# Kernel optimization log

Hardware: AMD Instinct MI355X
Metric: run time of the kernel (lower is better)

The kernel has to match this reference:

```python
import jax, jax.numpy as jnp
import numpy as np

SIZE = 784          # number of MPS sites (pixels)
D = 32              # bond dimension
EMB_D = 2           # local feature dim, embedding x -> [1-x, x]
NUM_LABELS = 10
LABEL_SITE = SIZE // 2
BATCH = 128
INIT_STD = 0.01     # matches default 'random_eye' init


def setup_inputs() -> dict:
    key = jax.random.key(0)
    k1, k2, k3 = jax.random.split(key, 3)
    # raw pixel values in [0,1] so the affine embedding is valid
    batch_input = jax.random.uniform(k1, (BATCH, SIZE), dtype=jnp.float32)
    eye = jnp.eye(D, dtype=jnp.float32)
    # 'random_eye' init: identity (broadcast over site & physical dims) + small noise.
    # Keeps the 784-long matrix chain numerically well-conditioned.
    core_tensors = eye[None, :, None, :] + INIT_STD * jax.random.normal(
        k2, (SIZE, D, EMB_D, D), dtype=jnp.float32)
    label_tensor = eye[:, None, :] + INIT_STD * jax.random.normal(
        k3, (D, NUM_LABELS, D), dtype=jnp.float32)
    return {"batch_input": batch_input,
            "core_tensors": core_tensors,
            "label_tensor": label_tensor}


def _chain_matmul(mats):
    """Ordered product M_0 @ M_1 @ ... @ M_{n-1} via log-depth pairwise tree.
    mats: [B, n, D, D] -> [B, D, D]. n is static, so the Python while is fine."""
    while mats.shape[1] > 1:
        n = mats.shape[1]
        half = n // 2
        prod = jnp.matmul(mats[:, 0:2 * half:2], mats[:, 1:2 * half:2])
        if n % 2:
            prod = jnp.concatenate([prod, mats[:, -1:]], axis=1)
        mats = prod
    return mats[:, 0]


def reference(batch_input, core_tensors, label_tensor):
    # embedding_map: x -> [1-x, x]                                  [B, S, d]
    emb = jnp.stack([1.0 - batch_input, batch_input], axis=-1)
    # _contract_batch_input: per-site matrices M[b,s] = sum_d core[s,:,d,:]*emb[b,s,d]
    mats = jnp.einsum('sadc,bsd->bsac', core_tensors, emb)       # [B, S, D, D]
    left = _chain_matmul(mats[:, :LABEL_SITE])                    # [B, D, D]
    right = _chain_matmul(mats[:, LABEL_SITE:])                   # [B, D, D]
    # periodic bc: out[b,l] = trace(left @ T_l @ right)
    return jnp.einsum('bij,jlk,bki->bl', left, label_tensor, right)  # [B, num_labels]
```

## Files before the change

kernel.cpp:

```cpp
#include <hip/hip_runtime.h>
#include <stdint.h>

typedef float f32x16 __attribute__((ext_vector_type(16)));
typedef short bf16x8 __attribute__((ext_vector_type(8)));
typedef uint32_t u32;
typedef uint32_t u32x4 __attribute__((ext_vector_type(4)));

#define SIZE 784
#define NLBL 10
#define LABEL_SITE 392
#define BATCH 128
#define PRE_ELEMS (SIZE * 2 * 64 * 4)


__device__ inline u32 cvt_pk(float a, float b) {
  u32 r;
  asm("v_cvt_pk_bf16_f32 %0, %1, %2" : "=v"(r) : "v"(a), "v"(b));
  return r;
}
__device__ inline float lo16f(u32 h) { return __uint_as_float(h << 16); }
__device__ inline float hi16f(u32 h) { return __uint_as_float(h & 0xffff0000u); }

__device__ inline void split_pack(const float s[8], u32 hi[4], u32 lo[4]) {
#pragma unroll
  for (int p = 0; p < 4; ++p) {
    u32 h = cvt_pk(s[2 * p], s[2 * p + 1]);
    hi[p] = h;
    lo[p] = cvt_pk(s[2 * p] - lo16f(h), s[2 * p + 1] - hi16f(h));
  }
}

__device__ inline f32x16 mfma_bb(const u32 (&a)[4], const u32 (&b)[4], f32x16 c) {
  union U { u32 u[4]; bf16x8 v; };
  U A, B;
#pragma unroll
  for (int i = 0; i < 4; ++i) { A.u[i] = a[i]; B.u[i] = b[i]; }
  return __builtin_amdgcn_mfma_f32_32x32x16_bf16(A.v, B.v, c, 0, 0, 0);
}
__device__ inline f32x16 mfma_v4(u32x4 a, const u32 (&b)[4], f32x16 c) {
  union UA { u32x4 u; bf16x8 v; } A; A.u = a;
  union UB { u32 u[4]; bf16x8 v; } B;
#pragma unroll
  for (int i = 0; i < 4; ++i) B.u[i] = b[i];
  return __builtin_amdgcn_mfma_f32_32x32x16_bf16(A.v, B.v, c, 0, 0, 0);
}

__device__ inline f32x16 ident_acc(int lane) {
  const int gam = lane & 31, hib = lane >> 5;
  f32x16 a;
#pragma unroll
  for (int reg = 0; reg < 16; ++reg) {
    int rho = (reg & 3) + 8 * (reg >> 2) + 4 * hib;
    a[reg] = (rho == gam) ? 1.0f : 0.0f;
  }
  return a;
}

__device__ inline void build_b(const f32x16& acc, int hib, int t,
                               u32 (&Bh)[4], u32 (&Bl)[4]) {
  float slot[8];
#pragma unroll
  for (int j = 0; j < 4; ++j) {
    const int q1 = 8 * t + j, q2 = q1 + 4;
    float z = hib ? acc[q1] : acc[q2];
    float wv = __shfl_xor(z, 32, 64);
    slot[j]     = hib ? wv : acc[q1];
    slot[j + 4] = hib ? acc[q2] : wv;
  }
  split_pack(slot, Bh, Bl);
}

__device__ inline f32x16 chain_step(const u32 (&Ah)[2][4], const u32 (&Al)[2][4],
                                    f32x16 acc, int hib) {
  f32x16 r;
#pragma unroll
  for (int q = 0; q < 16; ++q) r[q] = 0.0f;
#pragma unroll
  for (int t = 0; t < 2; ++t) {
    u32 Bh[4], Bl[4];
    build_b(acc, hib, t, Bh, Bl);
    r = mfma_bb(Al[t], Bh, r);
    r = mfma_bb(Ah[t], Bl, r);
    r = mfma_bb(Ah[t], Bh, r);
  }
  return r;
}

__device__ inline void store_afrag(float* dst, f32x16 acc, int lane) {
  const int gam = lane & 31, hib = lane >> 5;
  const int h = gam >> 4, j = gam & 7, b5 = (gam >> 3) & 1;
#pragma unroll
  for (int reg = 0; reg < 16; ++reg) {
    int rho = (reg & 3) + 8 * (reg >> 2) + 4 * hib;
    int lp = rho + 32 * b5;
    dst[h * 512 + lp * 8 + j] = acc[reg];
  }
}

__device__ inline void load_split_afrag(const float* src, int lane,
                                        u32 (&Ah)[2][4], u32 (&Al)[2][4]) {
#pragma unroll
  for (int h = 0; h < 2; ++h) {
    const float4* p = (const float4*)(src + h * 512 + lane * 8);
    float4 q0 = p[0], q1 = p[1];
    float v[8] = {q0.x, q0.y, q0.z, q0.w, q1.x, q1.y, q1.z, q1.w};
    split_pack(v, Ah[h], Al[h]);
  }
}

__global__ __launch_bounds__(256) void mps_precomp(const float* __restrict__ core,
                                                   u32* __restrict__ pc0h,
                                                   u32* __restrict__ pc0l,
                                                   u32* __restrict__ pdh,
                                                   u32* __restrict__ pdl) {
  const int tid = threadIdx.x;
  const int w = tid >> 6, lane = tid & 63;
  const int task = blockIdx.x * 4 + w;
  const int s = task >> 1, t = task & 1;
  const int r = lane & 31, hib = lane >> 5;
  const float* cs = core + (size_t)s * 2048 + r;
  u32 wc0h[4], wc0l[4], wdh[4], wdl[4];
#pragma unroll
  for (int p = 0; p < 4; ++p) {
    const int k0 = 16 * t + 8 * hib + 2 * p;
    float a0 = cs[k0 * 64],       a1 = cs[(k0 + 1) * 64];
    float b0 = cs[k0 * 64 + 32],  b1 = cs[(k0 + 1) * 64 + 32];
    float d0 = b0 - a0, d1 = b1 - a1;
    u32 h = cvt_pk(a0, a1);
    wc0h[p] = h;
    wc0l[p] = cvt_pk(a0 - lo16f(h), a1 - hi16f(h));
    u32 gg = cvt_pk(d0, d1);
    wdh[p] = gg;
    wdl[p] = cvt_pk(d0 - lo16f(gg), d1 - hi16f(gg));
  }
  const size_t base = ((size_t)task * 64 + lane) * 4;
  *(u32x4*)(pc0h + base) = *(u32x4*)wc0h;
  *(u32x4*)(pc0l + base) = *(u32x4*)wc0l;
  *(u32x4*)(pdh  + base) = *(u32x4*)wdh;
  *(u32x4*)(pdl  + base) = *(u32x4*)wdl;
}

__global__ __launch_bounds__(256, 4) void mps_phase1(
    const float* __restrict__ input,
    const u32* __restrict__ pc0h, const u32* __restrict__ pc0l,
    const u32* __restrict__ pdh,  const u32* __restrict__ pdl,
    float* __restrict__ wsA, int nseg, int seglen) {
  const int tid = threadIdx.x;
  const int w = tid >> 6, lane = tid & 63;
  const int hib = lane >> 5;
  const int g = blockIdx.x % nseg, c = blockIdx.x / nseg;
  const int bi = c * 4 + w;

  f32x16 acc = ident_acc(lane);
  f32x16 z16;
#pragma unroll
  for (int q = 0; q < 16; ++q) z16[q] = 0.0f;

  const int ci0 = g * seglen;
  for (int i = 0; i < seglen; ++i) {
    int s = LABEL_SITE + ci0 + i;
    if (s >= SIZE) s -= SIZE;
    const float x = input[(size_t)bi * SIZE + s];
    f32x16 rc = z16, rd = z16;
#pragma unroll
    for (int t = 0; t < 2; ++t) {
      const size_t base = ((size_t)(s * 2 + t) * 64 + lane) * 4;
      u32x4 Ac0h = *(const u32x4*)(pc0h + base);
      u32x4 Ac0l = *(const u32x4*)(pc0l + base);
      u32x4 Adh  = *(const u32x4*)(pdh + base);
      u32x4 Adl  = *(const u32x4*)(pdl + base);
      u32 Bh[4], Bl[4];
      build_b(acc, hib, t, Bh, Bl);
      rd = mfma_v4(Adl, Bh, rd);
      rd = mfma_v4(Adh, Bl, rd);
      rd = mfma_v4(Adh, Bh, rd);
      rc = mfma_v4(Ac0l, Bh, rc);
      rc = mfma_v4(Ac0h, Bl, rc);
      rc = mfma_v4(Ac0h, Bh, rc);
    }
#pragma unroll
    for (int q = 0; q < 16; ++q) acc[q] = fmaf(x, rd[q], rc[q]);
  }
  store_afrag(wsA + ((size_t)bi * nseg + g) * 1024, acc, lane);
}

__global__ __launch_bounds__(256) void mps_phase2a(const float* __restrict__ wsA,
                                                   float* __restrict__ wsB,
                                                   int nseg, int GG) {
  const int tid = threadIdx.x;
  const int w = tid >> 6, lane = tid & 63;
  const int wid = blockIdx.x * 4 + w;
  const int bi = wid & 127, gg = wid >> 7;
  f32x16 acc = ident_acc(lane);
  for (int g = gg * GG; g < gg * GG + GG; ++g) {
    u32 Ah[2][4], Al[2][4];
    load_split_afrag(wsA + ((size_t)bi * nseg + g) * 1024, lane, Ah, Al);
    acc = chain_step(Ah, Al, acc, lane >> 5);
  }
  store_afrag(wsB + ((size_t)bi * 7 + gg) * 1024, acc, lane);
}

__global__ __launch_bounds__(256) void mps_phase2b(const float* __restrict__ wsB,
                                                   const float* __restrict__ label,
                                                   float* __restrict__ out) {
  const int tid = threadIdx.x;
  const int w = tid >> 6, lane = tid & 63;
  const int bi = blockIdx.x * 4 + w;
  const int gam = lane & 31, hib = lane >> 5;
  f32x16 acc = ident_acc(lane);
  for (int gg = 0; gg < 7; ++gg) {
    u32 Ah[2][4], Al[2][4];
    load_split_afrag(wsB + ((size_t)bi * 7 + gg) * 1024, lane, Ah, Al);
    acc = chain_step(Ah, Al, acc, hib);
  }
  float part[NLBL];
#pragma unroll
  for (int l = 0; l < NLBL; ++l) part[l] = 0.0f;
#pragma unroll
  for (int reg = 0; reg < 16; ++reg) {
    const int rho = (reg & 3) + 8 * (reg >> 2) + 4 * hib;
    const float wv = acc[reg];
    const float* tp = label + rho * (NLBL * 32) + gam;
#pragma unroll
    for (int l = 0; l < NLBL; ++l) part[l] = fmaf(tp[l * 32], wv, part[l]);
  }
#pragma unroll
  for (int l = 0; l < NLBL; ++l) {
#pragma unroll
    for (int mask = 32; mask >= 1; mask >>= 1)
      part[l] += __shfl_xor(part[l], mask, 64);
  }
  if (lane == 0) {
#pragma unroll
    for (int l = 0; l < NLBL; ++l) out[bi * NLBL + l] = part[l];
  }
}

extern "C" void kernel_launch(void* const* d_in, const int* in_sizes, int n_in,
                              void* d_out, int out_size, void* d_ws, size_t ws_size,
                              hipStream_t stream) {
  const float* input = (const float*)d_in[0];
  const float* core  = (const float*)d_in[1];
  const float* label = (const float*)d_in[2];
  float* out = (float*)d_out;

  u32* pc0h = (u32*)d_ws;
  u32* pc0l = pc0h + PRE_ELEMS;
  u32* pdh  = pc0l + PRE_ELEMS;
  u32* pdl  = pdh + PRE_ELEMS;
  float* wsA = (float*)(pdl + PRE_ELEMS);

  const size_t need112 = ((size_t)4 * PRE_ELEMS + (size_t)BATCH * 112 * 1024 +
                          (size_t)BATCH * 7 * 1024) * 4;
  const int nseg = (ws_size >= need112) ? 112 : 56;
  const int seglen = SIZE / nseg;
  const int GG = nseg / 7;
  float* wsB = wsA + (size_t)BATCH * nseg * 1024;

  mps_precomp<<<dim3(392), dim3(256), 0, stream>>>(core, pc0h, pc0l, pdh, pdl);
  mps_phase1<<<dim3(nseg * 32), dim3(256), 0, stream>>>(input, pc0h, pc0l, pdh, pdl,
                                                        wsA, nseg, seglen);
  mps_phase2a<<<dim3(224), dim3(256), 0, stream>>>(wsA, wsB, nseg, GG);
  mps_phase2b<<<dim3(32), dim3(256), 0, stream>>>(wsB, label, out);
}
```

Measured before the change: 76.64 us.

## Process two batch rows per wave in phase1 and rebalance segment tree

Each phase1 wave now runs two batch elements' chains, loading the precomputed split core fragments once and using them for both, which halves the core-fragment traffic per chain. The segment count changes from 112 to 98, with groups of 7 in phase2a and 14 groups in phase2b, which changes the reduction tree shape and launch sizes. Intermediate matrices are now stored row-major and reloaded with a matching fragment loader. The risks are higher register pressure from two accumulators, fewer phase1 blocks, and longer serial chains per wave.

```diff
diff --git a/kernel.cpp b/kernel.cpp
--- a/kernel.cpp
+++ b/kernel.cpp
@@ -86,23 +86,23 @@
   return r;
 }
 
-__device__ inline void store_afrag(float* dst, f32x16 acc, int lane) {
+__device__ inline void store_cd(float* dst, f32x16 acc, int lane) {
   const int gam = lane & 31, hib = lane >> 5;
-  const int h = gam >> 4, j = gam & 7, b5 = (gam >> 3) & 1;
 #pragma unroll
   for (int reg = 0; reg < 16; ++reg) {
     int rho = (reg & 3) + 8 * (reg >> 2) + 4 * hib;
-    int lp = rho + 32 * b5;
-    dst[h * 512 + lp * 8 + j] = acc[reg];
-  }
-}
-
-__device__ inline void load_split_afrag(const float* src, int lane,
-                                        u32 (&Ah)[2][4], u32 (&Al)[2][4]) {
+    dst[rho * 32 + gam] = acc[reg];
+  }
+}
+
+__device__ inline void load_afrag_rm(const float* src, int lane,
+                                     u32 (&Ah)[2][4], u32 (&Al)[2][4]) {
+  const int row = lane & 31, hb8 = (lane >> 5) * 8;
 #pragma unroll
   for (int h = 0; h < 2; ++h) {
-    const float4* p = (const float4*)(src + h * 512 + lane * 8);
-    float4 q0 = p[0], q1 = p[1];
+    const float* p = src + row * 32 + h * 16 + hb8;
+    float4 q0 = *(const float4*)p;
+    float4 q1 = *(const float4*)(p + 4);
     float v[8] = {q0.x, q0.y, q0.z, q0.w, q1.x, q1.y, q1.z, q1.w};
     split_pack(v, Ah[h], Al[h]);
   }
@@ -149,68 +149,94 @@
   const int w = tid >> 6, lane = tid & 63;
   const int hib = lane >> 5;
   const int g = blockIdx.x % nseg, c = blockIdx.x / nseg;
-  const int bi = c * 4 + w;
-
-  f32x16 acc = ident_acc(lane);
-  f32x16 z16;
-#pragma unroll
-  for (int q = 0; q < 16; ++q) z16[q] = 0.0f;
-
+  const int bi0 = c * 8 + w * 2;
+
+  f32x16 acc0 = ident_acc(lane), acc1 = ident_acc(lane);
   const int ci0 = g * seglen;
   for (int i = 0; i < seglen; ++i) {
     int s = LABEL_SITE + ci0 + i;
     if (s >= SIZE) s -= SIZE;
-    const float x = input[(size_t)bi * SIZE + s];
-    f32x16 rc = z16, rd = z16;
+    const float x0 = input[(size_t)bi0 * SIZE + s];
+    const float x1 = input[(size_t)(bi0 + 1) * SIZE + s];
+    u32x4 C0h[2], C0l[2], Dh[2], Dl[2];
 #pragma unroll
     for (int t = 0; t < 2; ++t) {
       const size_t base = ((size_t)(s * 2 + t) * 64 + lane) * 4;
-      u32x4 Ac0h = *(const u32x4*)(pc0h + base);
-      u32x4 Ac0l = *(const u32x4*)(pc0l + base);
-      u32x4 Adh  = *(const u32x4*)(pdh + base);
-      u32x4 Adl  = *(const u32x4*)(pdl + base);
-      u32 Bh[4], Bl[4];
-      build_b(acc, hib, t, Bh, Bl);
-      rd = mfma_v4(Adl, Bh, rd);
-      rd = mfma_v4(Adh, Bl, rd);
-      rd = mfma_v4(Adh, Bh, rd);
-      rc = mfma_v4(Ac0l, Bh, rc);
-      rc = mfma_v4(Ac0h, Bl, rc);
-      rc = mfma_v4(Ac0h, Bh, rc);
+      C0h[t] = *(const u32x4*)(pc0h + base);
+      C0l[t] = *(const u32x4*)(pc0l + base);
+      Dh[t]  = *(const u32x4*)(pdh + base);
+      Dl[t]  = *(const u32x4*)(pdl + base);
     }
-#pragma unroll
-    for (int q = 0; q < 16; ++q) acc[q] = fmaf(x, rd[q], rc[q]);
-  }
-  store_afrag(wsA + ((size_t)bi * nseg + g) * 1024, acc, lane);
+    {
+      f32x16 rc, rd;
+#pragma unroll
+      for (int q = 0; q < 16; ++q) { rc[q] = 0.0f; rd[q] = 0.0f; }
+#pragma unroll
+      for (int t = 0; t < 2; ++t) {
+        u32 Bh[4], Bl[4];
+        build_b(acc0, hib, t, Bh, Bl);
+        rd = mfma_v4(Dl[t], Bh, rd);
+        rd = mfma_v4(Dh[t], Bl, rd);
+        rd = mfma_v4(Dh[t], Bh, rd);
+        rc = mfma_v4(C0l[t], Bh, rc);
+        rc = mfma_v4(C0h[t], Bl, rc);
+        rc = mfma_v4(C0h[t], Bh, rc);
+      }
+#pragma unroll
+      for (int q = 0; q < 16; ++q) acc0[q] = fmaf(x0, rd[q], rc[q]);
+    }
+    {
+      f32x16 rc, rd;
+#pragma unroll
+      for (int q = 0; q < 16; ++q) { rc[q] = 0.0f; rd[q] = 0.0f; }
+#pragma unroll
+      for (int t = 0; t < 2; ++t) {
+        u32 Bh[4], Bl[4];
+        build_b(acc1, hib, t, Bh, Bl);
+        rd = mfma_v4(Dl[t], Bh, rd);
+        rd = mfma_v4(Dh[t], Bl, rd);
+        rd = mfma_v4(Dh[t], Bh, rd);
+        rc = mfma_v4(C0l[t], Bh, rc);
+        rc = mfma_v4(C0h[t], Bl, rc);
+        rc = mfma_v4(C0h[t], Bh, rc);
+      }
+#pragma unroll
+      for (int q = 0; q < 16; ++q) acc1[q] = fmaf(x1, rd[q], rc[q]);
+    }
+  }
+  store_cd(wsA + ((size_t)bi0 * nseg + g) * 1024, acc0, lane);
+  store_cd(wsA + ((size_t)(bi0 + 1) * nseg + g) * 1024, acc1, lane);
 }
 
 __global__ __launch_bounds__(256) void mps_phase2a(const float* __restrict__ wsA,
                                                    float* __restrict__ wsB,
-                                                   int nseg, int GG) {
+                                                   int nseg) {
   const int tid = threadIdx.x;
   const int w = tid >> 6, lane = tid & 63;
   const int wid = blockIdx.x * 4 + w;
   const int bi = wid & 127, gg = wid >> 7;
   f32x16 acc = ident_acc(lane);
-  for (int g = gg * GG; g < gg * GG + GG; ++g) {
+  for (int g = gg * 7; g < gg * 7 + 7; ++g) {
     u32 Ah[2][4], Al[2][4];
-    load_split_afrag(wsA + ((size_t)bi * nseg + g) * 1024, lane, Ah, Al);
+    load_afrag_rm(wsA + ((size_t)bi * nseg + g) * 1024, lane, Ah, Al);
     acc = chain_step(Ah, Al, acc, lane >> 5);
   }
-  store_afrag(wsB + ((size_t)bi * 7 + gg) * 1024, acc, lane);
+  const int ngroups = nseg / 7;
+  store_cd(wsB + ((size_t)bi * ngroups + gg) * 1024, acc, lane);
 }
 
 __global__ __launch_bounds__(256) void mps_phase2b(const float* __restrict__ wsB,
                                                    const float* __restrict__ label,
-                                                   float* __restrict__ out) {
+                                                   float* __restrict__ out,
+                                                   int ngroups) {
   const int tid = threadIdx.x;
   const int w = tid >> 6, lane = tid & 63;
   const int bi = blockIdx.x * 4 + w;
   const int gam = lane & 31, hib = lane >> 5;
   f32x16 acc = ident_acc(lane);
-  for (int gg = 0; gg < 7; ++gg) {
+  for (int gg = 0; gg < ngroups; ++gg) {
     u32 Ah[2][4], Al[2][4];
-    load_split_afrag(wsB + ((size_t)bi * 7 + gg) * 1024, lane, Ah, Al);
+    load_afrag_rm(wsB + ((size_t)bi * ngroups + gg) * 1024, lane, Ah, Al);
     acc = chain_step(Ah, Al, acc, hib);
   }
   float part[NLBL];
@@ -250,16 +276,16 @@
   u32* pdl  = pdh + PRE_ELEMS;
   float* wsA = (float*)(pdl + PRE_ELEMS);
 
-  const size_t need112 = ((size_t)4 * PRE_ELEMS + (size_t)BATCH * 112 * 1024 +
-                          (size_t)BATCH * 7 * 1024) * 4;
-  const int nseg = (ws_size >= need112) ? 112 : 56;
+  const size_t need98 = ((size_t)4 * PRE_ELEMS + (size_t)BATCH * 98 * 1024 +
+                         (size_t)BATCH * 14 * 1024) * 4;
+  const int nseg = (ws_size >= need98) ? 98 : 56;
   const int seglen = SIZE / nseg;
-  const int GG = nseg / 7;
+  const int ngroups = nseg / 7;
   float* wsB = wsA + (size_t)BATCH * nseg * 1024;
 
   mps_precomp<<<dim3(392), dim3(256), 0, stream>>>(core, pc0h, pc0l, pdh, pdl);
-  mps_phase1<<<dim3(nseg * 32), dim3(256), 0, stream>>>(input, pc0h, pc0l, pdh, pdl,
+  mps_phase1<<<dim3(nseg * 16), dim3(256), 0, stream>>>(input, pc0h, pc0l, pdh, pdl,
                                                         wsA, nseg, seglen);
-  mps_phase2a<<<dim3(224), dim3(256), 0, stream>>>(wsA, wsB, nseg, GG);
-  mps_phase2b<<<dim3(32), dim3(256), 0, stream>>>(wsB, label, out);
-}
+  mps_phase2a<<<dim3(32 * ngroups), dim3(256), 0, stream>>>(wsA, wsB, nseg);
+  mps_phase2b<<<dim3(32), dim3(256), 0, stream>>>(wsB, label, out, ngroups);
+}
```

Result: slower. 83.98 us (+9.6%).

## Reshape phase-2 reduction into 7-wide groups and use row-major intermediates

Applied to the files above, without the earlier changes.

Phase 2a now reduces fixed groups of 7 segments, giving nseg/7 groups (16 when nseg is 112) and launching 32*ngroups blocks. Phase 2b then chains ngroups partial products instead of 7. This puts more warps on the first reduction stage and makes the serial tail longer. Intermediate matrices are stored in plain row-major layout and read back with row-strided float4 loads, and the occupancy hint of 4 is dropped from phase1's launch bounds.

```diff
diff --git a/kernel.cpp b/kernel.cpp
--- a/kernel.cpp
+++ b/kernel.cpp
@@ -86,23 +86,23 @@
   return r;
 }
 
-__device__ inline void store_afrag(float* dst, f32x16 acc, int lane) {
+__device__ inline void store_cd(float* dst, f32x16 acc, int lane) {
   const int gam = lane & 31, hib = lane >> 5;
-  const int h = gam >> 4, j = gam & 7, b5 = (gam >> 3) & 1;
 #pragma unroll
   for (int reg = 0; reg < 16; ++reg) {
     int rho = (reg & 3) + 8 * (reg >> 2) + 4 * hib;
-    int lp = rho + 32 * b5;
-    dst[h * 512 + lp * 8 + j] = acc[reg];
-  }
-}
-
-__device__ inline void load_split_afrag(const float* src, int lane,
-                                        u32 (&Ah)[2][4], u32 (&Al)[2][4]) {
+    dst[rho * 32 + gam] = acc[reg];
+  }
+}
+
+__device__ inline void load_afrag_rm(const float* src, int lane,
+                                     u32 (&Ah)[2][4], u32 (&Al)[2][4]) {
+  const int row = lane & 31, hb8 = (lane >> 5) * 8;
 #pragma unroll
   for (int h = 0; h < 2; ++h) {
-    const float4* p = (const float4*)(src + h * 512 + lane * 8);
-    float4 q0 = p[0], q1 = p[1];
+    const float* p = src + row * 32 + h * 16 + hb8;
+    float4 q0 = *(const float4*)p;
+    float4 q1 = *(const float4*)(p + 4);
     float v[8] = {q0.x, q0.y, q0.z, q0.w, q1.x, q1.y, q1.z, q1.w};
     split_pack(v, Ah[h], Al[h]);
   }
@@ -140,7 +140,7 @@
   *(u32x4*)(pdl  + base) = *(u32x4*)wdl;
 }
 
-__global__ __launch_bounds__(256, 4) void mps_phase1(
+__global__ __launch_bounds__(256) void mps_phase1(
     const float* __restrict__ input,
     const u32* __restrict__ pc0h, const u32* __restrict__ pc0l,
     const u32* __restrict__ pdh,  const u32* __restrict__ pdl,
@@ -152,65 +152,65 @@
   const int bi = c * 4 + w;
 
   f32x16 acc = ident_acc(lane);
-  f32x16 z16;
-#pragma unroll
-  for (int q = 0; q < 16; ++q) z16[q] = 0.0f;
-
   const int ci0 = g * seglen;
   for (int i = 0; i < seglen; ++i) {
     int s = LABEL_SITE + ci0 + i;
     if (s >= SIZE) s -= SIZE;
     const float x = input[(size_t)bi * SIZE + s];
-    f32x16 rc = z16, rd = z16;
+    f32x16 rc, rd;
+#pragma unroll
+    for (int q = 0; q < 16; ++q) { rc[q] = 0.0f; rd[q] = 0.0f; }
 #pragma unroll
     for (int t = 0; t < 2; ++t) {
       const size_t base = ((size_t)(s * 2 + t) * 64 + lane) * 4;
-      u32x4 Ac0h = *(const u32x4*)(pc0h + base);
-      u32x4 Ac0l = *(const u32x4*)(pc0l + base);
-      u32x4 Adh  = *(const u32x4*)(pdh + base);
-      u32x4 Adl  = *(const u32x4*)(pdl + base);
+      u32x4 C0h = *(const u32x4*)(pc0h + base);
+      u32x4 C0l = *(const u32x4*)(pc0l + base);
+      u32x4 Dh  = *(const u32x4*)(pdh + base);
+      u32x4 Dl  = *(const u32x4*)(pdl + base);
       u32 Bh[4], Bl[4];
       build_b(acc, hib, t, Bh, Bl);
-      rd = mfma_v4(Adl, Bh, rd);
-      rd = mfma_v4(Adh, Bl, rd);
-      rd = mfma_v4(Adh, Bh, rd);
-      rc = mfma_v4(Ac0l, Bh, rc);
-      rc = mfma_v4(Ac0h, Bl, rc);
-      rc = mfma_v4(Ac0h, Bh, rc);
+      rd = mfma_v4(Dl, Bh, rd);
+      rd = mfma_v4(Dh, Bl, rd);
+      rd = mfma_v4(Dh, Bh, rd);
+      rc = mfma_v4(C0l, Bh, rc);
+      rc = mfma_v4(C0h, Bl, rc);
+      rc = mfma_v4(C0h, Bh, rc);
     }
 #pragma unroll
     for (int q = 0; q < 16; ++q) acc[q] = fmaf(x, rd[q], rc[q]);
   }
-  store_afrag(wsA + ((size_t)bi * nseg + g) * 1024, acc, lane);
+  store_cd(wsA + ((size_t)bi * nseg + g) * 1024, acc, lane);
 }
 
 __global__ __launch_bounds__(256) void mps_phase2a(const float* __restrict__ wsA,
                                                    float* __restrict__ wsB,
-                                                   int nseg, int GG) {
+                                                   int nseg) {
   const int tid = threadIdx.x;
   const int w = tid >> 6, lane = tid & 63;
   const int wid = blockIdx.x * 4 + w;
   const int bi = wid & 127, gg = wid >> 7;
   f32x16 acc = ident_acc(lane);
-  for (int g = gg * GG; g < gg * GG + GG; ++g) {
+  for (int g = gg * 7; g < gg * 7 + 7; ++g) {
     u32 Ah[2][4], Al[2][4];
-    load_split_afrag(wsA + ((size_t)bi * nseg + g) * 1024, lane, Ah, Al);
+    load_afrag_rm(wsA + ((size_t)bi * nseg + g) * 1024, lane, Ah, Al);
     acc = chain_step(Ah, Al, acc, lane >> 5);
   }
-  store_afrag(wsB + ((size_t)bi * 7 + gg) * 1024, acc, lane);
+  const int ngroups = nseg / 7;
+  store_cd(wsB + ((size_t)bi * ngroups + gg) * 1024, acc, lane);
 }
 
 __global__ __launch_bounds__(256) void mps_phase2b(const float* __restrict__ wsB,
                                                    const float* __restrict__ label,
-                                                   float* __restrict__ out) {
+                                                   float* __restrict__ out,
+                                                   int ngroups) {
   const int tid = threadIdx.x;
   const int w = tid >> 6, lane = tid & 63;
   const int bi = blockIdx.x * 4 + w;
   const int gam = lane & 31, hib = lane >> 5;
   f32x16 acc = ident_acc(lane);
-  for (int gg = 0; gg < 7; ++gg) {
+  for (int gg = 0; gg < ngroups; ++gg) {
     u32 Ah[2][4], Al[2][4];
-    load_split_afrag(wsB + ((size_t)bi * 7 + gg) * 1024, lane, Ah, Al);
+    load_afrag_rm(wsB + ((size_t)bi * ngroups + gg) * 1024, lane, Ah, Al);
     acc = chain_step(Ah, Al, acc, hib);
   }
   float part[NLBL];
@@ -251,15 +251,15 @@
   float* wsA = (float*)(pdl + PRE_ELEMS);
 
   const size_t need112 = ((size_t)4 * PRE_ELEMS + (size_t)BATCH * 112 * 1024 +
-                          (size_t)BATCH * 7 * 1024) * 4;
+                          (size_t)BATCH * 16 * 1024) * 4;
   const int nseg = (ws_size >= need112) ? 112 : 56;
   const int seglen = SIZE / nseg;
-  const int GG = nseg / 7;
+  const int ngroups = nseg / 7;
   float* wsB = wsA + (size_t)BATCH * nseg * 1024;
 
   mps_precomp<<<dim3(392), dim3(256), 0, stream>>>(core, pc0h, pc0l, pdh, pdl);
   mps_phase1<<<dim3(nseg * 32), dim3(256), 0, stream>>>(input, pc0h, pc0l, pdh, pdl,
                                                         wsA, nseg, seglen);
-  mps_phase2a<<<dim3(224), dim3(256), 0, stream>>>(wsA, wsB, nseg, GG);
-  mps_phase2b<<<dim3(32), dim3(256), 0, stream>>>(wsB, label, out);
-}
+  mps_phase2a<<<dim3(32 * ngroups), dim3(256), 0, stream>>>(wsA, wsB, nseg);
+  mps_phase2b<<<dim3(32), dim3(256), 0, stream>>>(wsB, label, out, ngroups);
+}
```

Result: slower. 86.87 us (+13.3%).
